# Performance work log

Measured on AMD Instinct MI355X. Metric: run time of the kernel, lower is better.

Reference implementation:

```python
import jax, jax.numpy as jnp
import numpy as np

N = 1_000_000   # total nodes
B = 1024        # number of graphs
H = 64          # node feature dim / LSTM hidden
STEPS = 5       # Set2Set processing steps
PROJ = 128      # projection_dim


def setup_inputs() -> dict:
    key = jax.random.key(0)
    ks = jax.random.split(key, 12)
    x = jax.random.normal(ks[0], (N, H), dtype=jnp.float32)
    batch = jnp.sort(jax.random.randint(ks[1], (N,), 0, B)).astype(jnp.int64)
    s = 1.0 / np.sqrt(H)
    # torch.nn.LSTM(input_size=2H, hidden_size=H), gate order i,f,g,o
    W_ih = jax.random.uniform(ks[2], (4 * H, 2 * H), minval=-s, maxval=s, dtype=jnp.float32)
    W_hh = jax.random.uniform(ks[3], (4 * H, H), minval=-s, maxval=s, dtype=jnp.float32)
    b_ih = jax.random.uniform(ks[4], (4 * H,), minval=-s, maxval=s, dtype=jnp.float32)
    b_hh = jax.random.uniform(ks[5], (4 * H,), minval=-s, maxval=s, dtype=jnp.float32)
    s1 = 1.0 / np.sqrt(2 * H)
    W1 = jax.random.uniform(ks[6], (256, 2 * H), minval=-s1, maxval=s1, dtype=jnp.float32)
    b1 = jax.random.uniform(ks[7], (256,), minval=-s1, maxval=s1, dtype=jnp.float32)
    s2 = 1.0 / np.sqrt(256)
    W2 = jax.random.uniform(ks[8], (PROJ, 256), minval=-s2, maxval=s2, dtype=jnp.float32)
    b2 = jax.random.uniform(ks[9], (PROJ,), minval=-s2, maxval=s2, dtype=jnp.float32)
    return {"x": x, "batch": batch, "W_ih": W_ih, "W_hh": W_hh, "b_ih": b_ih,
            "b_hh": b_hh, "W1": W1, "b1": b1, "W2": W2, "b2": b2}


def _set2set(x, batch, W_ih, W_hh, b_ih, b_hh):
    q_star = jnp.zeros((B, 2 * H), x.dtype)
    h = jnp.zeros((B, H), x.dtype)
    c = jnp.zeros((B, H), x.dtype)
    for _ in range(STEPS):
        gates = q_star @ W_ih.T + b_ih + h @ W_hh.T + b_hh
        i, f, g, o = jnp.split(gates, 4, axis=-1)
        i = jax.nn.sigmoid(i); f = jax.nn.sigmoid(f)
        g = jnp.tanh(g); o = jax.nn.sigmoid(o)
        c = f * c + i * g
        h = o * jnp.tanh(c)
        q = h  # [B, H]
        # segment-wise attention over ragged node sets
        e = jnp.sum(x * q[batch], axis=-1)                         # [N]
        emax = jax.ops.segment_max(e, batch, num_segments=B)       # [B]
        a = jnp.exp(e - emax[batch])
        denom = jax.ops.segment_sum(a, batch, num_segments=B)
        a = a / jnp.maximum(denom, 1e-16)[batch]
        r = jax.ops.segment_sum(a[:, None] * x, batch, num_segments=B)  # [B, H]
        q_star = jnp.concatenate([q, r], axis=-1)
    return q_star


def reference(x, batch, W_ih, W_hh, b_ih, b_hh, W1, b1, W2, b2):
    out = _set2set(x, batch, W_ih, W_hh, b_ih, b_hh)   # [B, 2H]
    out = out @ W1.T + b1                               # [B, 256]
    out = jax.nn.relu(out) @ W2.T + b2                  # [B, PROJ]
    return out
```

## Files before the change

### kernel.cpp

```cpp
#include <hip/hip_runtime.h>
#include <float.h>
#include <math.h>

#define NB 1024
#define HD 64
#define NSTEPS 5

__device__ __forceinline__ float sigmoidf_(float x) {
    return 1.0f / (1.0f + __expf(-x));
}

__global__ void seg_bounds_kernel(const int* __restrict__ batch,
                                  int* __restrict__ seg_start, int n) {
    int i = blockIdx.x * blockDim.x + threadIdx.x;
    if (i >= n) return;
    int b = batch[i];
    if (i == 0) {
        for (int j = 0; j <= b; ++j) seg_start[j] = 0;
    } else {
        int pb = batch[i - 1];
        for (int j = pb + 1; j <= b; ++j) seg_start[j] = i;
    }
    if (i == n - 1) {
        for (int j = b + 1; j <= NB; ++j) seg_start[j] = n;
    }
}

__device__ __forceinline__ void async_ld16(const float* g, float* l) {
    __builtin_amdgcn_global_load_lds(
        (const __attribute__((address_space(1))) void*)g,
        (__attribute__((address_space(3))) void*)l, 16, 0, 0);
}

__global__ __launch_bounds__(512, 4) void set2set_fused_kernel(
    const float* __restrict__ x,
    const int* __restrict__ seg,
    const float* __restrict__ W_ih,
    const float* __restrict__ W_hh,
    const float* __restrict__ b_ih,
    const float* __restrict__ b_hh,
    const float* __restrict__ W1,
    const float* __restrict__ b1,
    const float* __restrict__ W2,
    const float* __restrict__ b2,
    float* __restrict__ out)
{
    __shared__ __align__(16) float sbuf[8][2][16 * HD];
    __shared__ __align__(16) float hs[HD], cs[HD], rs[HD];
    __shared__ __align__(16) float gates[256], gpart[256];
    __shared__ __align__(16) float lr[8][HD];
    __shared__ float lm[8], ls[8];

    const int b = blockIdx.x;
    const int tid = threadIdx.x;
    const int lane = tid & 63;
    const int wv = tid >> 6;
    const int fc = lane & 15;
    const int grp = lane >> 4;

    const int s0 = seg[b], e0 = seg[b + 1];
    const int len = e0 - s0;
    const int ntiles = (len + 15) >> 4;
    const int maxidx4 = e0 * 16 - 1;

    if (tid < HD) { hs[tid] = 0.0f; cs[tid] = 0.0f; rs[tid] = 0.0f; }
    __syncthreads();

    for (int step = 0; step < NSTEPS; ++step) {
        if (wv < ntiles) {
            const int tb4 = (s0 + wv * 16) * 16;
            float* dst = &sbuf[wv][0][0];
#pragma unroll
            for (int i = 0; i < 4; ++i) {
                int g4 = min(tb4 + i * 64 + lane, maxidx4);
                async_ld16(x + (size_t)g4 * 4, dst + i * 256);
            }
        }

        if (step == 0) {
            if (tid < 256) gates[tid] = b_ih[tid] + b_hh[tid];
        } else {
            float acc = 0.0f;
            if (tid < 256) {
                acc = b_ih[tid] + b_hh[tid];
                const float4* w = (const float4*)(W_ih + tid * 128);
                const float4* hq = (const float4*)hs;
                const float4* rq = (const float4*)rs;
#pragma unroll
                for (int k = 0; k < 16; ++k) {
                    float4 ww = w[k]; float4 v = hq[k];
                    acc = fmaf(ww.x, v.x, acc); acc = fmaf(ww.y, v.y, acc);
                    acc = fmaf(ww.z, v.z, acc); acc = fmaf(ww.w, v.w, acc);
                }
#pragma unroll
                for (int k = 0; k < 16; ++k) {
                    float4 ww = w[16 + k]; float4 v = rq[k];
                    acc = fmaf(ww.x, v.x, acc); acc = fmaf(ww.y, v.y, acc);
                    acc = fmaf(ww.z, v.z, acc); acc = fmaf(ww.w, v.w, acc);
                }
            } else {
                int j = tid - 256;
                float a2 = 0.0f;
                const float4* w = (const float4*)(W_hh + j * 64);
                const float4* hq = (const float4*)hs;
#pragma unroll
                for (int k = 0; k < 16; ++k) {
                    float4 ww = w[k]; float4 v = hq[k];
                    a2 = fmaf(ww.x, v.x, a2); a2 = fmaf(ww.y, v.y, a2);
                    a2 = fmaf(ww.z, v.z, a2); a2 = fmaf(ww.w, v.w, a2);
                }
                gpart[j] = a2;
            }
            __syncthreads();
            if (tid < 256) gates[tid] = acc + gpart[tid];
        }
        __syncthreads();

        if (tid < HD) {
            float ig = sigmoidf_(gates[tid]);
            float fg = sigmoidf_(gates[tid + 64]);
            float gg = tanhf(gates[tid + 128]);
            float og = sigmoidf_(gates[tid + 192]);
            float cp = (step == 0) ? 0.0f : cs[tid];
            float cn = fmaf(fg, cp, ig * gg);
            cs[tid] = cn;
            hs[tid] = og * tanhf(cn);
        }
        __syncthreads();

        float4 q4 = *(const float4*)(hs + fc * 4);
        float m = -FLT_MAX, sum = 0.0f;
        float4 r4 = make_float4(0.0f, 0.0f, 0.0f, 0.0f);

        int cur = 0;
        for (int t = wv; t < ntiles; t += 8) {
            __builtin_amdgcn_sched_barrier(0);
            int nxt = t + 8;
            if (nxt < ntiles) {
                const int tb4 = (s0 + nxt * 16) * 16;
                float* dst = &sbuf[wv][cur ^ 1][0];
#pragma unroll
                for (int i = 0; i < 4; ++i) {
                    int g4 = min(tb4 + i * 64 + lane, maxidx4);
                    async_ld16(x + (size_t)g4 * 4, dst + i * 256);
                }
                asm volatile("s_waitcnt vmcnt(4)" ::: "memory");
            } else {
                asm volatile("s_waitcnt vmcnt(0)" ::: "memory");
            }
            __builtin_amdgcn_sched_barrier(0);

            const float* buf = &sbuf[wv][cur][0];
            const int nbase = t * 16;
#pragma unroll
            for (int u = 0; u < 4; ++u) {
                int nl = u * 4 + grp;
                float4 xv = *(const float4*)(buf + nl * 64 + fc * 4);
                float d = xv.x * q4.x;
                d = fmaf(xv.y, q4.y, d);
                d = fmaf(xv.z, q4.z, d);
                d = fmaf(xv.w, q4.w, d);
                d += __shfl_xor(d, 1);
                d += __shfl_xor(d, 2);
                d += __shfl_xor(d, 4);
                d += __shfl_xor(d, 8);
                bool valid = (nbase + nl) < len;
                float eeff = valid ? d : -FLT_MAX;
                float nm = fmaxf(m, eeff);
                float sc = __expf(m - nm);
                float w = valid ? __expf(eeff - nm) : 0.0f;
                sum = fmaf(sum, sc, w);
                r4.x = fmaf(r4.x, sc, w * xv.x);
                r4.y = fmaf(r4.y, sc, w * xv.y);
                r4.z = fmaf(r4.z, sc, w * xv.z);
                r4.w = fmaf(r4.w, sc, w * xv.w);
                m = nm;
            }
            cur ^= 1;
        }

#pragma unroll
        for (int off = 16; off < 64; off <<= 1) {
            float om = __shfl_xor(m, off);
            float os = __shfl_xor(sum, off);
            float ox = __shfl_xor(r4.x, off);
            float oy = __shfl_xor(r4.y, off);
            float oz = __shfl_xor(r4.z, off);
            float ow = __shfl_xor(r4.w, off);
            float nm = fmaxf(m, om);
            float s1 = __expf(m - nm);
            float s2 = __expf(om - nm);
            sum = sum * s1 + os * s2;
            r4.x = r4.x * s1 + ox * s2;
            r4.y = r4.y * s1 + oy * s2;
            r4.z = r4.z * s1 + oz * s2;
            r4.w = r4.w * s1 + ow * s2;
            m = nm;
        }
        if (lane < 16) {
            if (lane == 0) { lm[wv] = m; ls[wv] = sum; }
            *(float4*)&lr[wv][lane * 4] = r4;
        }
        __syncthreads();

        if (tid < HD) {
            float M = lm[0];
#pragma unroll
            for (int w = 1; w < 8; ++w) M = fmaxf(M, lm[w]);
            float S = 0.0f, rf = 0.0f;
#pragma unroll
            for (int w = 0; w < 8; ++w) {
                float ww = __expf(lm[w] - M);
                S = fmaf(ls[w], ww, S);
                rf = fmaf(lr[w][tid], ww, rf);
            }
            rs[tid] = rf / fmaxf(S, 1e-16f);
        }
        __syncthreads();
    }

    if (tid < 256) {
        float acc = b1[tid];
        const float4* w = (const float4*)(W1 + tid * 128);
        const float4* hq = (const float4*)hs;
        const float4* rq = (const float4*)rs;
#pragma unroll
        for (int k = 0; k < 16; ++k) {
            float4 ww = w[k]; float4 v = hq[k];
            acc = fmaf(ww.x, v.x, acc); acc = fmaf(ww.y, v.y, acc);
            acc = fmaf(ww.z, v.z, acc); acc = fmaf(ww.w, v.w, acc);
        }
#pragma unroll
        for (int k = 0; k < 16; ++k) {
            float4 ww = w[16 + k]; float4 v = rq[k];
            acc = fmaf(ww.x, v.x, acc); acc = fmaf(ww.y, v.y, acc);
            acc = fmaf(ww.z, v.z, acc); acc = fmaf(ww.w, v.w, acc);
        }
        gates[tid] = fmaxf(acc, 0.0f);
    }
    __syncthreads();
    if (tid < 128) {
        float acc = b2[tid];
        const float4* w = (const float4*)(W2 + tid * 256);
        const float4* hq = (const float4*)gates;
#pragma unroll 8
        for (int k = 0; k < 64; ++k) {
            float4 ww = w[k]; float4 v = hq[k];
            acc = fmaf(ww.x, v.x, acc); acc = fmaf(ww.y, v.y, acc);
            acc = fmaf(ww.z, v.z, acc); acc = fmaf(ww.w, v.w, acc);
        }
        out[b * 128 + tid] = acc;
    }
}

extern "C" void kernel_launch(void* const* d_in, const int* in_sizes, int n_in,
                              void* d_out, int out_size, void* d_ws, size_t ws_size,
                              hipStream_t stream) {
    const float* x     = (const float*)d_in[0];
    const int*   batch = (const int*)d_in[1];
    const float* W_ih  = (const float*)d_in[2];
    const float* W_hh  = (const float*)d_in[3];
    const float* b_ih  = (const float*)d_in[4];
    const float* b_hh  = (const float*)d_in[5];
    const float* W1    = (const float*)d_in[6];
    const float* b1    = (const float*)d_in[7];
    const float* W2    = (const float*)d_in[8];
    const float* b2    = (const float*)d_in[9];
    float* out = (float*)d_out;
    const int N = in_sizes[1];

    int* seg = (int*)d_ws;

    seg_bounds_kernel<<<(N + 255) / 256, 256, 0, stream>>>(batch, seg, N);
    set2set_fused_kernel<<<NB, 512, 0, stream>>>(x, seg, W_ih, W_hh, b_ih, b_hh,
                                                 W1, b1, W2, b2, out);
}
```

Before: 561.9 us.

## Cache node features in registers across Set2Set steps instead of reloading

Each wave now loads its share of the segment's x tiles (up to 9 tiles per wave) into registers once before the step loop and reuses them across all 5 Set2Set steps. This replaces the per-step LDS double-buffered async loads with global reloads only for overflow tiles. It also splits the online softmax into 4 independent accumulator chains that are merged afterwards, which shortens the serial dependency. The cost is a much higher register count, so launch bounds drop to 2 blocks per SM and occupancy falls. Long segments that exceed the register cache still reload from global memory without prefetch.

```diff
diff --git a/kernel.cpp b/kernel.cpp
--- a/kernel.cpp
+++ b/kernel.cpp
@@ -5,6 +5,7 @@
 #define NB 1024
 #define HD 64
 #define NSTEPS 5
+#define RT 9
 
 __device__ __forceinline__ float sigmoidf_(float x) {
     return 1.0f / (1.0f + __expf(-x));
@@ -26,13 +27,30 @@
     }
 }
 
-__device__ __forceinline__ void async_ld16(const float* g, float* l) {
-    __builtin_amdgcn_global_load_lds(
-        (const __attribute__((address_space(1))) void*)g,
-        (__attribute__((address_space(3))) void*)l, 16, 0, 0);
-}
-
-__global__ __launch_bounds__(512, 4) void set2set_fused_kernel(
+#define ONLINE_UPD(U, XV, NODE)                                         \
+    {                                                                   \
+        float d = (XV).x * q4.x;                                        \
+        d = fmaf((XV).y, q4.y, d);                                      \
+        d = fmaf((XV).z, q4.z, d);                                      \
+        d = fmaf((XV).w, q4.w, d);                                      \
+        d += __shfl_xor(d, 1);                                          \
+        d += __shfl_xor(d, 2);                                          \
+        d += __shfl_xor(d, 4);                                          \
+        d += __shfl_xor(d, 8);                                          \
+        bool valid = (NODE) < len;                                      \
+        float eeff = valid ? d : -FLT_MAX;                              \
+        float nm = fmaxf(mm[U], eeff);                                  \
+        float sc = __expf(mm[U] - nm);                                  \
+        float w = valid ? __expf(eeff - nm) : 0.0f;                     \
+        ss[U] = fmaf(ss[U], sc, w);                                     \
+        rr[U].x = fmaf(rr[U].x, sc, w * (XV).x);                        \
+        rr[U].y = fmaf(rr[U].y, sc, w * (XV).y);                        \
+        rr[U].z = fmaf(rr[U].z, sc, w * (XV).z);                        \
+        rr[U].w = fmaf(rr[U].w, sc, w * (XV).w);                        \
+        mm[U] = nm;                                                     \
+    }
+
+__global__ __launch_bounds__(512, 2) void set2set_fused_kernel(
     const float* __restrict__ x,
     const int* __restrict__ seg,
     const float* __restrict__ W_ih,
@@ -45,7 +63,6 @@
     const float* __restrict__ b2,
     float* __restrict__ out)
 {
-    __shared__ __align__(16) float sbuf[8][2][16 * HD];
     __shared__ __align__(16) float hs[HD], cs[HD], rs[HD];
     __shared__ __align__(16) float gates[256], gpart[256];
     __shared__ __align__(16) float lr[8][HD];
@@ -63,20 +80,24 @@
     const int ntiles = (len + 15) >> 4;
     const int maxidx4 = e0 * 16 - 1;
 
+    float4 xr[4 * RT];
+#pragma unroll
+    for (int j = 0; j < RT; ++j) {
+        int t = wv + 8 * j;
+        if (t < ntiles) {
+            int tb4 = (s0 + t * 16) * 16;
+#pragma unroll
+            for (int u = 0; u < 4; ++u) {
+                int g4 = min(tb4 + u * 64 + lane, maxidx4);
+                xr[4 * j + u] = *(const float4*)(x + (size_t)g4 * 4);
+            }
+        }
+    }
+
     if (tid < HD) { hs[tid] = 0.0f; cs[tid] = 0.0f; rs[tid] = 0.0f; }
     __syncthreads();
 
     for (int step = 0; step < NSTEPS; ++step) {
-        if (wv < ntiles) {
-            const int tb4 = (s0 + wv * 16) * 16;
-            float* dst = &sbuf[wv][0][0];
-#pragma unroll
-            for (int i = 0; i < 4; ++i) {
-                int g4 = min(tb4 + i * 64 + lane, maxidx4);
-                async_ld16(x + (size_t)g4 * 4, dst + i * 256);
-            }
-        }
-
         if (step == 0) {
             if (tid < 256) gates[tid] = b_ih[tid] + b_hh[tid];
         } else {
@@ -129,56 +150,50 @@
         __syncthreads();
 
         float4 q4 = *(const float4*)(hs + fc * 4);
-        float m = -FLT_MAX, sum = 0.0f;
-        float4 r4 = make_float4(0.0f, 0.0f, 0.0f, 0.0f);
-
-        int cur = 0;
-        for (int t = wv; t < ntiles; t += 8) {
-            __builtin_amdgcn_sched_barrier(0);
-            int nxt = t + 8;
-            if (nxt < ntiles) {
-                const int tb4 = (s0 + nxt * 16) * 16;
-                float* dst = &sbuf[wv][cur ^ 1][0];
-#pragma unroll
-                for (int i = 0; i < 4; ++i) {
-                    int g4 = min(tb4 + i * 64 + lane, maxidx4);
-                    async_ld16(x + (size_t)g4 * 4, dst + i * 256);
-                }
-                asm volatile("s_waitcnt vmcnt(4)" ::: "memory");
-            } else {
-                asm volatile("s_waitcnt vmcnt(0)" ::: "memory");
-            }
-            __builtin_amdgcn_sched_barrier(0);
-
-            const float* buf = &sbuf[wv][cur][0];
-            const int nbase = t * 16;
+        float mm[4], ss[4];
+        float4 rr[4];
+#pragma unroll
+        for (int u = 0; u < 4; ++u) {
+            mm[u] = -FLT_MAX; ss[u] = 0.0f;
+            rr[u] = make_float4(0.0f, 0.0f, 0.0f, 0.0f);
+        }
+
+#pragma unroll
+        for (int j = 0; j < RT; ++j) {
+            int t = wv + 8 * j;
+            if (t < ntiles) {
+                int nbase = t * 16;
+                ONLINE_UPD(0, xr[4 * j + 0], nbase + 0 * 4 + grp);
+                ONLINE_UPD(1, xr[4 * j + 1], nbase + 1 * 4 + grp);
+                ONLINE_UPD(2, xr[4 * j + 2], nbase + 2 * 4 + grp);
+                ONLINE_UPD(3, xr[4 * j + 3], nbase + 3 * 4 + grp);
+            }
+        }
+        for (int t = 8 * RT + wv; t < ntiles; t += 8) {
+            int tb4 = (s0 + t * 16) * 16;
+            int nbase = t * 16;
 #pragma unroll
             for (int u = 0; u < 4; ++u) {
-                int nl = u * 4 + grp;
-                float4 xv = *(const float4*)(buf + nl * 64 + fc * 4);
-                float d = xv.x * q4.x;
-                d = fmaf(xv.y, q4.y, d);
-                d = fmaf(xv.z, q4.z, d);
-                d = fmaf(xv.w, q4.w, d);
-                d += __shfl_xor(d, 1);
-                d += __shfl_xor(d, 2);
-                d += __shfl_xor(d, 4);
-                d += __shfl_xor(d, 8);
-                bool valid = (nbase + nl) < len;
-                float eeff = valid ? d : -FLT_MAX;
-                float nm = fmaxf(m, eeff);
-                float sc = __expf(m - nm);
-                float w = valid ? __expf(eeff - nm) : 0.0f;
-                sum = fmaf(sum, sc, w);
-                r4.x = fmaf(r4.x, sc, w * xv.x);
-                r4.y = fmaf(r4.y, sc, w * xv.y);
-                r4.z = fmaf(r4.z, sc, w * xv.z);
-                r4.w = fmaf(r4.w, sc, w * xv.w);
-                m = nm;
-            }
-            cur ^= 1;
-        }
-
+                int g4 = min(tb4 + u * 64 + lane, maxidx4);
+                float4 xv = *(const float4*)(x + (size_t)g4 * 4);
+                ONLINE_UPD(u, xv, nbase + u * 4 + grp);
+            }
+        }
+
+        float m = mm[0], sum = ss[0];
+        float4 r4 = rr[0];
+#pragma unroll
+        for (int u = 1; u < 4; ++u) {
+            float nm = fmaxf(m, mm[u]);
+            float s1 = __expf(m - nm);
+            float s2 = __expf(mm[u] - nm);
+            sum = sum * s1 + ss[u] * s2;
+            r4.x = r4.x * s1 + rr[u].x * s2;
+            r4.y = r4.y * s1 + rr[u].y * s2;
+            r4.z = r4.z * s1 + rr[u].z * s2;
+            r4.w = r4.w * s1 + rr[u].w * s2;
+            m = nm;
+        }
 #pragma unroll
         for (int off = 16; off < 64; off <<= 1) {
             float om = __shfl_xor(m, off);
```

After: 598.3 us. 6.5% more time.

## Cache each graph's node features in registers and LDS across all steps

Applied to the files above, without the earlier changes.

Instead of streaming x from global memory on every Set2Set step, each block loads its segment once. Each thread keeps one node's 64 features in registers, and a further 576 nodes go into swizzled LDS. Attention now uses a two-pass max, then exp-sum and a weighted sum per thread-node, with a butterfly transpose-reduce across lanes and a global-memory fallback for overflow nodes. This removes four of the five passes over x. The costs are heavy register and LDS use, occupancy pinned to 2 waves per EU, and recomputing dot products for overflow nodes in three passes.

```diff
diff --git a/kernel.cpp b/kernel.cpp
--- a/kernel.cpp
+++ b/kernel.cpp
@@ -5,6 +5,8 @@
 #define NB 1024
 #define HD 64
 #define NSTEPS 5
+#define LN 576
+#define LTILES 36
 
 __device__ __forceinline__ float sigmoidf_(float x) {
     return 1.0f / (1.0f + __expf(-x));
@@ -32,7 +34,30 @@
         (__attribute__((address_space(3))) void*)l, 16, 0, 0);
 }
 
-__global__ __launch_bounds__(512, 4) void set2set_fused_kernel(
+__device__ __forceinline__ float dot4(float4 a, float4 b) {
+    float d = a.x * b.x;
+    d = fmaf(a.y, b.y, d);
+    d = fmaf(a.z, b.z, d);
+    return fmaf(a.w, b.w, d);
+}
+__device__ __forceinline__ float4 shfl_xor4(float4 v, int m) {
+    return make_float4(__shfl_xor(v.x, m), __shfl_xor(v.y, m),
+                       __shfl_xor(v.z, m), __shfl_xor(v.w, m));
+}
+__device__ __forceinline__ float4 add4(float4 a, float4 b) {
+    return make_float4(a.x + b.x, a.y + b.y, a.z + b.z, a.w + b.w);
+}
+__device__ __forceinline__ float4 sfma4(float a, float4 v, float4 c) {
+    return make_float4(fmaf(a, v.x, c.x), fmaf(a, v.y, c.y),
+                       fmaf(a, v.z, c.z), fmaf(a, v.w, c.w));
+}
+__device__ __forceinline__ float4 smul4(float a, float4 v) {
+    return make_float4(a * v.x, a * v.y, a * v.z, a * v.w);
+}
+
+__global__ __attribute__((amdgpu_flat_work_group_size(512, 512)))
+__attribute__((amdgpu_waves_per_eu(2, 2)))
+void set2set_fused_kernel(
     const float* __restrict__ x,
     const int* __restrict__ seg,
     const float* __restrict__ W_ih,
@@ -45,7 +70,7 @@
     const float* __restrict__ b2,
     float* __restrict__ out)
 {
-    __shared__ __align__(16) float sbuf[8][2][16 * HD];
+    __shared__ __align__(16) float xl[LN * HD];
     __shared__ __align__(16) float hs[HD], cs[HD], rs[HD];
     __shared__ __align__(16) float gates[256], gpart[256];
     __shared__ __align__(16) float lr[8][HD];
@@ -55,28 +80,40 @@
     const int tid = threadIdx.x;
     const int lane = tid & 63;
     const int wv = tid >> 6;
-    const int fc = lane & 15;
-    const int grp = lane >> 4;
+    const int lg = tid;
 
     const int s0 = seg[b], e0 = seg[b + 1];
     const int len = e0 - s0;
-    const int ntiles = (len + 15) >> 4;
-    const int maxidx4 = e0 * 16 - 1;
-
+    const int maxidx4 = max(e0 * 16 - 1, 0);
+
+    float4 x1[16];
+    {
+        int nd = (len > 0) ? (s0 + min(lg, len - 1)) : 0;
+        const float* gp = x + (size_t)nd * 64;
+#pragma unroll
+        for (int k = 0; k < 16; ++k) x1[k] = *(const float4*)(gp + k * 4);
+    }
+    for (int t = wv; t < LTILES; t += 8) {
+        if (512 + t * 16 >= len) break;
+#pragma unroll
+        for (int u = 0; u < 4; ++u) {
+            int node = 512 + t * 16 + u * 4 + (lane >> 4);
+            int ksrc = (lane & 15) ^ (node & 7);
+            int g4 = min((s0 + node) * 16 + ksrc, maxidx4);
+            async_ld16(x + (size_t)g4 * 4, xl + t * 1024 + u * 256);
+        }
+    }
+    asm volatile("s_waitcnt vmcnt(0)" ::: "memory");
     if (tid < HD) { hs[tid] = 0.0f; cs[tid] = 0.0f; rs[tid] = 0.0f; }
     __syncthreads();
 
+    const bool v1  = lg < len;
+    const bool vl1 = (512 + lg) < len;
+    const bool vl2 = (wv == 0) && ((1024 + lane) < len);
+    const int  sw1 = lg & 7;
+    const int  sw2 = lane & 7;
+
     for (int step = 0; step < NSTEPS; ++step) {
-        if (wv < ntiles) {
-            const int tb4 = (s0 + wv * 16) * 16;
-            float* dst = &sbuf[wv][0][0];
-#pragma unroll
-            for (int i = 0; i < 4; ++i) {
-                int g4 = min(tb4 + i * 64 + lane, maxidx4);
-                async_ld16(x + (size_t)g4 * 4, dst + i * 256);
-            }
-        }
-
         if (step == 0) {
             if (tid < 256) gates[tid] = b_ih[tid] + b_hh[tid];
         } else {
@@ -87,35 +124,22 @@
                 const float4* hq = (const float4*)hs;
                 const float4* rq = (const float4*)rs;
 #pragma unroll
-                for (int k = 0; k < 16; ++k) {
-                    float4 ww = w[k]; float4 v = hq[k];
-                    acc = fmaf(ww.x, v.x, acc); acc = fmaf(ww.y, v.y, acc);
-                    acc = fmaf(ww.z, v.z, acc); acc = fmaf(ww.w, v.w, acc);
-                }
-#pragma unroll
-                for (int k = 0; k < 16; ++k) {
-                    float4 ww = w[16 + k]; float4 v = rq[k];
-                    acc = fmaf(ww.x, v.x, acc); acc = fmaf(ww.y, v.y, acc);
-                    acc = fmaf(ww.z, v.z, acc); acc = fmaf(ww.w, v.w, acc);
-                }
+                for (int k = 0; k < 16; ++k) acc += dot4(w[k], hq[k]);
+#pragma unroll
+                for (int k = 0; k < 16; ++k) acc += dot4(w[16 + k], rq[k]);
             } else {
                 int j = tid - 256;
                 float a2 = 0.0f;
                 const float4* w = (const float4*)(W_hh + j * 64);
                 const float4* hq = (const float4*)hs;
 #pragma unroll
-                for (int k = 0; k < 16; ++k) {
-                    float4 ww = w[k]; float4 v = hq[k];
-                    a2 = fmaf(ww.x, v.x, a2); a2 = fmaf(ww.y, v.y, a2);
-                    a2 = fmaf(ww.z, v.z, a2); a2 = fmaf(ww.w, v.w, a2);
-                }
+                for (int k = 0; k < 16; ++k) a2 += dot4(w[k], hq[k]);
                 gpart[j] = a2;
             }
             __syncthreads();
             if (tid < 256) gates[tid] = acc + gpart[tid];
         }
         __syncthreads();
-
         if (tid < HD) {
             float ig = sigmoidf_(gates[tid]);
             float fg = sigmoidf_(gates[tid + 64]);
@@ -128,92 +152,146 @@
         }
         __syncthreads();
 
-        float4 q4 = *(const float4*)(hs + fc * 4);
-        float m = -FLT_MAX, sum = 0.0f;
-        float4 r4 = make_float4(0.0f, 0.0f, 0.0f, 0.0f);
-
-        int cur = 0;
-        for (int t = wv; t < ntiles; t += 8) {
-            __builtin_amdgcn_sched_barrier(0);
-            int nxt = t + 8;
-            if (nxt < ntiles) {
-                const int tb4 = (s0 + nxt * 16) * 16;
-                float* dst = &sbuf[wv][cur ^ 1][0];
-#pragma unroll
-                for (int i = 0; i < 4; ++i) {
-                    int g4 = min(tb4 + i * 64 + lane, maxidx4);
-                    async_ld16(x + (size_t)g4 * 4, dst + i * 256);
+        float d1a = 0.f, d1b = 0.f, la = 0.f, lb = 0.f;
+#pragma unroll
+        for (int k = 0; k < 16; ++k) {
+            float4 q4 = *(const float4*)(hs + k * 4);
+            float dv = dot4(x1[k], q4);
+            float lv = dot4(*(const float4*)(xl + lg * 64 + ((k ^ sw1) << 2)), q4);
+            if (k & 1) { d1b += dv; lb += lv; } else { d1a += dv; la += lv; }
+        }
+        float d2a = 0.f, d2b = 0.f;
+        if (wv == 0) {
+#pragma unroll
+            for (int k = 0; k < 16; ++k) {
+                float4 q4 = *(const float4*)(hs + k * 4);
+                float lv = dot4(*(const float4*)(xl + (512 + lane) * 64 + ((k ^ sw2) << 2)), q4);
+                if (k & 1) d2b += lv; else d2a += lv;
+            }
+        }
+        float e1  = v1  ? (d1a + d1b) : -FLT_MAX;
+        float el1 = vl1 ? (la + lb)   : -FLT_MAX;
+        float el2 = vl2 ? (d2a + d2b) : -FLT_MAX;
+        float ml = fmaxf(fmaxf(e1, el1), el2);
+        for (int nb = 1088 + lg; nb < len; nb += 512) {
+            const float* gp = x + (size_t)(s0 + nb) * 64;
+            float da = 0.f, db = 0.f;
+#pragma unroll
+            for (int k = 0; k < 16; ++k) {
+                float dv = dot4(*(const float4*)(gp + k * 4), *(const float4*)(hs + k * 4));
+                if (k & 1) db += dv; else da += dv;
+            }
+            ml = fmaxf(ml, da + db);
+        }
+#pragma unroll
+        for (int off = 1; off < 64; off <<= 1) ml = fmaxf(ml, __shfl_xor(ml, off));
+        if (lane == 0) lm[wv] = ml;
+        __syncthreads();
+        float M = lm[0];
+#pragma unroll
+        for (int w = 1; w < 8; ++w) M = fmaxf(M, lm[w]);
+
+        float a1  = v1  ? __expf(e1 - M)  : 0.f;
+        float al1 = vl1 ? __expf(el1 - M) : 0.f;
+        float al2 = vl2 ? __expf(el2 - M) : 0.f;
+        float s_lane = a1 + al1 + al2;
+        for (int nb = 1088 + lg; nb < len; nb += 512) {
+            const float* gp = x + (size_t)(s0 + nb) * 64;
+            float da = 0.f, db = 0.f;
+#pragma unroll
+            for (int k = 0; k < 16; ++k) {
+                float dv = dot4(*(const float4*)(gp + k * 4), *(const float4*)(hs + k * 4));
+                if (k & 1) db += dv; else da += dv;
+            }
+            s_lane += __expf(da + db - M);
+        }
+        float sw_ = s_lane;
+#pragma unroll
+        for (int off = 1; off < 64; off <<= 1) sw_ += __shfl_xor(sw_, off);
+        if (lane == 0) ls[wv] = sw_;
+
+#pragma unroll
+        for (int h = 0; h < 2; ++h) {
+            float4 r8[8];
+#pragma unroll
+            for (int j = 0; j < 8; ++j) r8[j] = smul4(a1, x1[h * 8 + j]);
+#pragma unroll
+            for (int j = 0; j < 8; ++j) {
+                int k = h * 8 + j;
+                float4 lv = *(const float4*)(xl + lg * 64 + ((k ^ sw1) << 2));
+                r8[j] = sfma4(al1, lv, r8[j]);
+            }
+            if (wv == 0) {
+#pragma unroll
+                for (int j = 0; j < 8; ++j) {
+                    int k = h * 8 + j;
+                    float4 lv = *(const float4*)(xl + (512 + lane) * 64 + ((k ^ sw2) << 2));
+                    r8[j] = sfma4(al2, lv, r8[j]);
                 }
-                asm volatile("s_waitcnt vmcnt(4)" ::: "memory");
-            } else {
-                asm volatile("s_waitcnt vmcnt(0)" ::: "memory");
-            }
-            __builtin_amdgcn_sched_barrier(0);
-
-            const float* buf = &sbuf[wv][cur][0];
-            const int nbase = t * 16;
-#pragma unroll
-            for (int u = 0; u < 4; ++u) {
-                int nl = u * 4 + grp;
-                float4 xv = *(const float4*)(buf + nl * 64 + fc * 4);
-                float d = xv.x * q4.x;
-                d = fmaf(xv.y, q4.y, d);
-                d = fmaf(xv.z, q4.z, d);
-                d = fmaf(xv.w, q4.w, d);
-                d += __shfl_xor(d, 1);
-                d += __shfl_xor(d, 2);
-                d += __shfl_xor(d, 4);
-                d += __shfl_xor(d, 8);
-                bool valid = (nbase + nl) < len;
-                float eeff = valid ? d : -FLT_MAX;
-                float nm = fmaxf(m, eeff);
-                float sc = __expf(m - nm);
-                float w = valid ? __expf(eeff - nm) : 0.0f;
-                sum = fmaf(sum, sc, w);
-                r4.x = fmaf(r4.x, sc, w * xv.x);
-                r4.y = fmaf(r4.y, sc, w * xv.y);
-                r4.z = fmaf(r4.z, sc, w * xv.z);
-                r4.w = fmaf(r4.w, sc, w * xv.w);
-                m = nm;
-            }
-            cur ^= 1;
-        }
-
-#pragma unroll
-        for (int off = 16; off < 64; off <<= 1) {
-            float om = __shfl_xor(m, off);
-            float os = __shfl_xor(sum, off);
-            float ox = __shfl_xor(r4.x, off);
-            float oy = __shfl_xor(r4.y, off);
-            float oz = __shfl_xor(r4.z, off);
-            float ow = __shfl_xor(r4.w, off);
-            float nm = fmaxf(m, om);
-            float s1 = __expf(m - nm);
-            float s2 = __expf(om - nm);
-            sum = sum * s1 + os * s2;
-            r4.x = r4.x * s1 + ox * s2;
-            r4.y = r4.y * s1 + oy * s2;
-            r4.z = r4.z * s1 + oz * s2;
-            r4.w = r4.w * s1 + ow * s2;
-            m = nm;
-        }
-        if (lane < 16) {
-            if (lane == 0) { lm[wv] = m; ls[wv] = sum; }
-            *(float4*)&lr[wv][lane * 4] = r4;
+            }
+            for (int nb = 1088 + lg; nb < len; nb += 512) {
+                const float* gp = x + (size_t)(s0 + nb) * 64;
+                float da = 0.f, db = 0.f;
+#pragma unroll
+                for (int k = 0; k < 16; ++k) {
+                    float dv = dot4(*(const float4*)(gp + k * 4), *(const float4*)(hs + k * 4));
+                    if (k & 1) db += dv; else da += dv;
+                }
+                float a = __expf(da + db - M);
+#pragma unroll
+                for (int j = 0; j < 8; ++j)
+                    r8[j] = sfma4(a, *(const float4*)(gp + (h * 8 + j) * 4), r8[j]);
+            }
+            {
+                bool s = lane & 32;
+#pragma unroll
+                for (int j = 0; j < 4; ++j) {
+                    float4 kp = s ? r8[j + 4] : r8[j];
+                    float4 sd = s ? r8[j] : r8[j + 4];
+                    r8[j] = add4(kp, shfl_xor4(sd, 32));
+                }
+            }
+            {
+                bool s = lane & 16;
+#pragma unroll
+                for (int j = 0; j < 2; ++j) {
+                    float4 kp = s ? r8[j + 2] : r8[j];
+                    float4 sd = s ? r8[j] : r8[j + 2];
+                    r8[j] = add4(kp, shfl_xor4(sd, 16));
+                }
+            }
+            {
+                bool s = lane & 8;
+                float4 kp = s ? r8[1] : r8[0];
+                float4 sd = s ? r8[0] : r8[1];
+                r8[0] = add4(kp, shfl_xor4(sd, 8));
+            }
+            float p0, p1;
+            {
+                bool s = lane & 4;
+                p0 = s ? r8[0].z : r8[0].x;
+                p1 = s ? r8[0].w : r8[0].y;
+                float q0 = s ? r8[0].x : r8[0].z;
+                float q1 = s ? r8[0].y : r8[0].w;
+                p0 += __shfl_xor(q0, 4);
+                p1 += __shfl_xor(q1, 4);
+            }
+            float pv;
+            {
+                bool s = lane & 2;
+                pv = s ? p1 : p0;
+                float sd = s ? p0 : p1;
+                pv += __shfl_xor(sd, 2);
+            }
+            pv += __shfl_xor(pv, 1);
+            if (!(lane & 1)) lr[wv][h * 32 + ((lane >> 1) & 31)] = pv;
         }
         __syncthreads();
 
         if (tid < HD) {
-            float M = lm[0];
-#pragma unroll
-            for (int w = 1; w < 8; ++w) M = fmaxf(M, lm[w]);
-            float S = 0.0f, rf = 0.0f;
-#pragma unroll
-            for (int w = 0; w < 8; ++w) {
-                float ww = __expf(lm[w] - M);
-                S = fmaf(ls[w], ww, S);
-                rf = fmaf(lr[w][tid], ww, rf);
-            }
+            float S = 0.f, rf = 0.f;
+#pragma unroll
+            for (int w = 0; w < 8; ++w) { S += ls[w]; rf += lr[w][tid]; }
             rs[tid] = rf / fmaxf(S, 1e-16f);
         }
         __syncthreads();
@@ -225,17 +303,9 @@
         const float4* hq = (const float4*)hs;
         const float4* rq = (const float4*)rs;
 #pragma unroll
-        for (int k = 0; k < 16; ++k) {
-            float4 ww = w[k]; float4 v = hq[k];
-            acc = fmaf(ww.x, v.x, acc); acc = fmaf(ww.y, v.y, acc);
-            acc = fmaf(ww.z, v.z, acc); acc = fmaf(ww.w, v.w, acc);
-        }
-#pragma unroll
-        for (int k = 0; k < 16; ++k) {
-            float4 ww = w[16 + k]; float4 v = rq[k];
-            acc = fmaf(ww.x, v.x, acc); acc = fmaf(ww.y, v.y, acc);
-            acc = fmaf(ww.z, v.z, acc); acc = fmaf(ww.w, v.w, acc);
-        }
+        for (int k = 0; k < 16; ++k) acc += dot4(w[k], hq[k]);
+#pragma unroll
+        for (int k = 0; k < 16; ++k) acc += dot4(w[16 + k], rq[k]);
         gates[tid] = fmaxf(acc, 0.0f);
     }
     __syncthreads();
@@ -244,11 +314,7 @@
         const float4* w = (const float4*)(W2 + tid * 256);
         const float4* hq = (const float4*)gates;
 #pragma unroll 8
-        for (int k = 0; k < 64; ++k) {
-            float4 ww = w[k]; float4 v = hq[k];
-            acc = fmaf(ww.x, v.x, acc); acc = fmaf(ww.y, v.y, acc);
-            acc = fmaf(ww.z, v.z, acc); acc = fmaf(ww.w, v.w, acc);
-        }
+        for (int k = 0; k < 64; ++k) acc += dot4(w[k], hq[k]);
         out[b * 128 + tid] = acc;
     }
 }
```

After: 680.2 us. +21.1%, slower.
